# Kernel optimization log

Hardware: AMD Instinct MI355X
Metric: run time of the kernel (lower is better)

The kernel has to match this reference:

```python
import jax, jax.numpy as jnp
import numpy as np

VOXEL_SIZE = 0.4
STRIDE = 2
NUM_BATCH = 4
PRE_MAXSIZE = 1024  # nms_premaxsize
NMS_THR = 0.1
NEG_INF = -1e9


def setup_inputs() -> dict:
    key = jax.random.key(0)
    ks = jax.random.split(key, 7)
    N, C = 200000, 256
    feat = jax.random.normal(ks[0], (N, C), dtype=jnp.float32)
    batch_idx = jax.random.randint(ks[1], (N,), 0, NUM_BATCH, dtype=jnp.int32)
    coor = jax.random.randint(ks[2], (N, 2), 0, 400, dtype=jnp.int32)
    W_cls = jax.random.normal(ks[3], (C, 2), dtype=jnp.float32) * 0.02
    b_cls = jnp.zeros((2,), dtype=jnp.float32)
    W_reg = jax.random.normal(ks[4], (C, 9), dtype=jnp.float32) * 0.02
    b_reg = jnp.zeros((9,), dtype=jnp.float32)
    return {"feat": feat, "batch_idx": batch_idx, "coor": coor,
            "W_cls": W_cls, "b_cls": b_cls, "W_reg": W_reg, "b_reg": b_reg}


def _bev_iou(bx):
    # bx: [K,7] (x,y,z,l,w,h,r); axis-aligned BEV IoU on (x,y,l,w)
    x, y, l, w = bx[:, 0], bx[:, 1], bx[:, 3], bx[:, 4]
    x1, x2 = x - l / 2, x + l / 2
    y1, y2 = y - w / 2, y + w / 2
    ix = jnp.maximum(jnp.minimum(x2[:, None], x2[None, :]) - jnp.maximum(x1[:, None], x1[None, :]), 0.0)
    iy = jnp.maximum(jnp.minimum(y2[:, None], y2[None, :]) - jnp.maximum(y1[:, None], y1[None, :]), 0.0)
    inter = ix * iy
    area = l * w
    union = area[:, None] + area[None, :] - inter
    return inter / jnp.maximum(union, 1e-6)


def _nms_keep(iou):
    # greedy NMS over score-descending rows; returns keep mask [K]
    K = iou.shape[0]
    idx = jnp.arange(K)

    def body(i, supp):
        keep_i = jnp.logical_not(supp[i])
        new = keep_i & (iou[i] > NMS_THR) & (idx > i)
        return supp | new

    supp = jax.lax.fori_loop(0, K, body, jnp.zeros((K,), dtype=bool))
    return jnp.logical_not(supp)


def reference(feat, batch_idx, coor, W_cls, b_cls, W_reg, b_reg):
    # ---- shared heads over all sparse voxels ----
    cls_logits = feat @ W_cls + b_cls            # [N, 1+1] (neg evidence, class)
    probs = jax.nn.softmax(cls_logits, axis=-1)
    cls_prob = probs[:, 1:]                      # [N, n_cls]
    conf = jnp.max(cls_prob, axis=-1)            # [N]
    label = jnp.argmax(cls_prob, axis=-1)        # [N]

    reg = feat @ W_reg + b_reg                   # [N, 9] -> ctr(3) dim(3) dir(2) scr(1)
    ctr, dim, drn, scr = reg[:, :3], reg[:, 3:6], reg[:, 6:8], reg[:, 8]
    scr = jax.nn.sigmoid(scr)                    # sigmoid_keys=['scr']

    # indices2metric: voxel indices -> metric centers
    centers = coor.astype(jnp.float32) * (VOXEL_SIZE * STRIDE)  # [N, 2]

    xy = centers + ctr[:, :2]
    z = ctr[:, 2]
    lwh = jnp.exp(jnp.clip(dim, -6.0, 6.0))
    angle = jnp.arctan2(drn[:, 0], drn[:, 1])
    boxes = jnp.concatenate([xy, z[:, None], lwh, angle[:, None]], axis=-1)  # [N, 7]
    score = conf * scr                           # [N]

    def per_sample(b):
        s = jnp.where(batch_idx == b, score, NEG_INF)
        vals, idx = jax.lax.top_k(s, PRE_MAXSIZE)          # score-sorted (desc)
        bx = boxes[idx]                                     # [K, 7]
        lb = label[idx]                                     # [K]
        valid = vals > NEG_INF / 2
        iou = _bev_iou(bx)
        keep = _nms_keep(iou) & valid
        out = jnp.concatenate([bx, vals[:, None]], axis=-1) * keep[:, None]  # [K, 8]
        return out, lb, keep

    out, lb, keep = jax.vmap(per_sample)(jnp.arange(NUM_BATCH))
    return out, lb, keep
```

## Files before the change

### kernel.cpp

```cpp
#include <hip/hip_runtime.h>
#include <math.h>

#define NBATCH 4
#define PRE 1024
#define CAND 4096
#define NHIST 65536
#define MAXSLOT 384

typedef __attribute__((address_space(1))) const void GlbVoid;
typedef __attribute__((address_space(3))) void LdsVoid;

__device__ __forceinline__ void gld_lds16(const void* g, void* l) {
    __builtin_amdgcn_global_load_lds((GlbVoid*)g, (LdsVoid*)l, 16, 0, 0);
}

__device__ __forceinline__ unsigned long long allow_mask(int i, int l) {
    int base = l << 6;
    if (i < base) return ~0ull;
    int sh = i - base + 1;
    if (sh >= 64) return 0ull;
    return (~0ull) << sh;
}

__global__ void k0_weights(const float* __restrict__ Wcls, const float* __restrict__ bcls,
                           const float* __restrict__ Wreg, const float* __restrict__ breg,
                           double* __restrict__ Wd3, float* __restrict__ Wf8,
                           double* __restrict__ biasD, float* __restrict__ biasF) {
    int j = blockIdx.x;
    int c = threadIdx.x;
    if (j < 2) {
        Wd3[j * 256 + c] = (double)Wcls[c * 2 + j];
        if (c == 0) biasD[j] = (double)bcls[j];
    } else if (j == 10) {
        Wd3[2 * 256 + c] = (double)Wreg[c * 9 + 8];
        if (c == 0) biasD[2] = (double)breg[8];
    } else {
        int r = j - 2;
        Wf8[r * 256 + c] = Wreg[c * 9 + r];
        if (c == 0) biasF[r] = breg[r];
    }
}

__global__ __launch_bounds__(256) void k1_points(
    const float* __restrict__ feat, const int* __restrict__ batch_idx,
    const int* __restrict__ coor, const double* __restrict__ Wd3,
    const float* __restrict__ Wf8, const double* __restrict__ biasD,
    const float* __restrict__ biasF, float* __restrict__ pointData,
    unsigned long long* __restrict__ keys, unsigned int* __restrict__ hist, int N) {
    __shared__ float sbuf[2][256 * 32];
    const int tid = threadIdx.x;
    const int w = tid >> 6, lane = tid & 63;
    const int p0 = blockIdx.x * 256;

    double accD0 = 0.0, accD1 = 0.0, accD2 = 0.0;
    float accF[8];
#pragma unroll
    for (int j = 0; j < 8; ++j) accF[j] = 0.f;

    const int s_src = (lane & 7) ^ (lane >> 3);

    auto stage = [&](int buf, int ch) {
#pragma unroll
        for (int it = 0; it < 8; ++it) {
            int R0 = w * 64 + it * 8;
            int r = R0 + (lane >> 3);
            int gp = p0 + r;
            if (gp >= N) gp = N - 1;
            const float* g = feat + (size_t)gp * 256 + ch * 32 + s_src * 4;
            gld_lds16(g, &sbuf[buf][R0 * 32]);
        }
    };

    auto compute = [&](int buf, int ch) {
        const float* row = &sbuf[buf][tid * 32];
        const int rs = tid & 7;
#pragma unroll
        for (int k4 = 0; k4 < 8; ++k4) {
            const float4 v = *(const float4*)(row + ((k4 ^ rs) * 4));
            const int cb = ch * 32 + k4 * 4;
            float vv[4] = {v.x, v.y, v.z, v.w};
#pragma unroll
            for (int m = 0; m < 4; ++m) {
                int c = cb + m;
                double fd = (double)vv[m];
                accD0 = fma(fd, Wd3[c], accD0);
                accD1 = fma(fd, Wd3[256 + c], accD1);
                accD2 = fma(fd, Wd3[512 + c], accD2);
#pragma unroll
                for (int j = 0; j < 8; ++j) accF[j] = fmaf(vv[m], Wf8[j * 256 + c], accF[j]);
            }
        }
    };

    stage(0, 0);
    __syncthreads();
    for (int ch = 0; ch < 8; ++ch) {
        if (ch < 7) stage((ch + 1) & 1, ch + 1);
        compute(ch & 1, ch);
        __syncthreads();
    }

    int gp = p0 + tid;
    if (gp < N) {
        double d0 = biasD[0] + accD0, d1 = biasD[1] + accD1, d2 = biasD[2] + accD2;
        float f[8];
#pragma unroll
        for (int j = 0; j < 8; ++j) f[j] = biasF[j] + accF[j];
        double conf = 1.0 / (1.0 + exp(-(d1 - d0)));
        double scr = 1.0 / (1.0 + exp(-d2));
        double score = conf * scr;
        float s32 = (float)score;

        float cx = (float)coor[2 * gp] * 0.8f;
        float cy = (float)coor[2 * gp + 1] * 0.8f;
        float bx = cx + f[0], by = cy + f[1], bz = f[2];
        float bl = expf(fminf(fmaxf(f[3], -6.f), 6.f));
        float bw = expf(fminf(fmaxf(f[4], -6.f), 6.f));
        float bh = expf(fminf(fmaxf(f[5], -6.f), 6.f));
        float ba = atan2f(f[6], f[7]);

        float4* pd = (float4*)(pointData + (size_t)gp * 8);
        pd[0] = make_float4(bx, by, bz, bl);
        pd[1] = make_float4(bw, bh, ba, s32);
        keys[gp] = (unsigned long long)__double_as_longlong(score);
        int b = batch_idx[gp];
        atomicAdd(&hist[b * NHIST + (__float_as_uint(s32) >> 16)], 1u);
    }
}

__global__ __launch_bounds__(256) void k2_thresh(const unsigned int* __restrict__ hist,
                                                 unsigned int* __restrict__ Tarr) {
    int b = blockIdx.x, tid = threadIdx.x;
    __shared__ unsigned int csum[256];
    __shared__ unsigned int chunkv[256];
    __shared__ int stc;
    __shared__ unsigned int scum;
    const unsigned int* h = hist + b * NHIST;
    unsigned int s = 0;
    for (int m = 0; m < 256; ++m) s += h[tid * 256 + m];
    csum[tid] = s;
    __syncthreads();
    if (tid == 0) {
        unsigned int cum = 0; int tc = -1;
        for (int t = 255; t >= 0; --t) {
            if (cum + csum[t] >= 1024u) { tc = t; break; }
            cum += csum[t];
        }
        stc = tc; scum = cum;
    }
    __syncthreads();
    int tc = stc;
    if (tc < 0) { if (tid == 0) Tarr[b] = 0u; return; }
    chunkv[tid] = h[tc * 256 + tid];
    __syncthreads();
    if (tid == 0) {
        unsigned int cum = scum, T = (unsigned int)(tc * 256);
        for (int m = 255; m >= 0; --m) {
            unsigned int c = chunkv[m];
            if (cum + c >= 1024u) { T = (unsigned int)(tc * 256 + m); break; }
            cum += c;
        }
        Tarr[b] = T;
    }
}

__global__ void k3_compact(const int* __restrict__ batch_idx, const float* __restrict__ pointData,
                           const unsigned long long* __restrict__ keys,
                           const unsigned int* __restrict__ Tarr, unsigned int* __restrict__ candCount,
                           unsigned int* __restrict__ candIdx, unsigned long long* __restrict__ candKey,
                           int N) {
    int p = blockIdx.x * 256 + threadIdx.x;
    if (p >= N) return;
    int b = batch_idx[p];
    float s32 = pointData[(size_t)p * 8 + 7];
    unsigned int bucket = __float_as_uint(s32) >> 16;
    if (bucket >= Tarr[b]) {
        unsigned int pos = atomicAdd(&candCount[b], 1u);
        if (pos < CAND) {
            candIdx[b * CAND + pos] = (unsigned int)p;
            candKey[b * CAND + pos] = keys[p];
        }
    }
}

__global__ __launch_bounds__(1024) void k4_sort(const unsigned int* __restrict__ candCount,
                                                const unsigned int* __restrict__ candIdx,
                                                const unsigned long long* __restrict__ candKey,
                                                const float* __restrict__ pointData,
                                                float* __restrict__ topBox,
                                                unsigned int* __restrict__ validArr) {
    int b = blockIdx.x, tid = threadIdx.x;
    __shared__ unsigned long long ka[CAND];
    __shared__ unsigned int id[CAND];
    unsigned int cnt = candCount[b];
    if (cnt > CAND) cnt = CAND;
    int n = (cnt <= 2048u) ? 2048 : 4096;
    for (int t = tid; t < n; t += 1024) {
        if ((unsigned int)t < cnt) {
            ka[t] = ~candKey[b * CAND + t];
            id[t] = candIdx[b * CAND + t];
        } else {
            ka[t] = ~0ull;
            id[t] = 0xFFFFFFFFu;
        }
    }
    __syncthreads();
    for (int k = 2; k <= n; k <<= 1) {
        for (int j = k >> 1; j > 0; j >>= 1) {
            for (int t = tid; t < n; t += 1024) {
                int l = t ^ j;
                if (l > t) {
                    bool up = ((t & k) == 0);
                    unsigned long long kt = ka[t], kl = ka[l];
                    unsigned int it_ = id[t], il = id[l];
                    bool gt = (kt > kl) || (kt == kl && it_ > il);
                    if (gt == up) { ka[t] = kl; ka[l] = kt; id[t] = il; id[l] = it_; }
                }
            }
            __syncthreads();
        }
    }
    unsigned int gi = id[tid];
    bool valid = (gi != 0xFFFFFFFFu) && ((unsigned int)tid < cnt);
    float v[8];
#pragma unroll
    for (int k = 0; k < 8; ++k) v[k] = 0.f;
    if (valid) {
        const float* pd = pointData + (size_t)gi * 8;
#pragma unroll
        for (int k = 0; k < 8; ++k) v[k] = pd[k];
    }
    float* tb = topBox + (size_t)(b * PRE + tid) * 8;
#pragma unroll
    for (int k = 0; k < 8; ++k) tb[k] = v[k];
    validArr[b * PRE + tid] = valid ? 1u : 0u;
}

__global__ __launch_bounds__(256) void k5_iou(const float* __restrict__ topBox,
                                              unsigned long long* __restrict__ M) {
    int wid = blockIdx.x * 4 + (threadIdx.x >> 6);
    int lane = threadIdx.x & 63;
    int b = wid >> 14;
    int rem = wid & 16383;
    int i = rem >> 4;
    int wj = rem & 15;
    if (wj < (i >> 6)) return;
    const float* bi = topBox + (size_t)(b * PRE + i) * 8;
    int j = wj * 64 + lane;
    const float* bj = topBox + (size_t)(b * PRE + j) * 8;
    float xi = bi[0], yi = bi[1], li = bi[3], wi_ = bi[4];
    float xj = bj[0], yj = bj[1], lj = bj[3], wj_ = bj[4];
    float x1i = xi - li * 0.5f, x2i = xi + li * 0.5f;
    float y1i = yi - wi_ * 0.5f, y2i = yi + wi_ * 0.5f;
    float x1j = xj - lj * 0.5f, x2j = xj + lj * 0.5f;
    float y1j = yj - wj_ * 0.5f, y2j = yj + wj_ * 0.5f;
    float ix = fmaxf(fminf(x2i, x2j) - fmaxf(x1i, x1j), 0.0f);
    float iy = fmaxf(fminf(y2i, y2j) - fmaxf(y1i, y1j), 0.0f);
    float inter = ix * iy;
    float ai = li * wi_, aj = lj * wj_;
    float uni = ai + aj - inter;
    float iou = inter / fmaxf(uni, 1e-6f);
    unsigned long long m = __ballot(iou > 0.1f);
    if (lane == 0) M[(size_t)(b * PRE + i) * 16 + wj] = m;
}

__global__ __launch_bounds__(256) void k6_nms(const unsigned long long* __restrict__ M,
                                              const unsigned int* __restrict__ validArr,
                                              const float* __restrict__ topBox,
                                              float* __restrict__ out0,
                                              float* __restrict__ keepOut) {
    __shared__ unsigned long long Mc[MAXSLOT * 16];
    __shared__ unsigned int slotIdx[PRE];
    __shared__ unsigned int cntSh;
    __shared__ unsigned long long suppSh[16];
    int b = blockIdx.x, tid = threadIdx.x;
    if (tid == 0) cntSh = 0;
    __syncthreads();
    for (int r = tid; r < PRE; r += 256) {
        const unsigned long long* row = M + (size_t)(b * PRE + r) * 16;
        unsigned long long w[16];
        unsigned long long o = 0ull;
#pragma unroll
        for (int l = 0; l < 16; ++l) { w[l] = row[l] & allow_mask(r, l); o |= w[l]; }
        unsigned int s = 0xFFFFFFFFu;
        if (o != 0ull) {
            unsigned int slot = atomicAdd(&cntSh, 1u);
            if (slot < MAXSLOT) {
                s = slot;
#pragma unroll
                for (int l = 0; l < 16; ++l) Mc[slot * 16 + l] = w[l];
            } else s = 0xFFFFFFFEu;
        }
        slotIdx[r] = s;
    }
    __syncthreads();
    if (tid < 64) {
        int lane = tid;
        unsigned long long supp = 0ull;
        for (int g = 0; g < 16; ++g) {
            unsigned long long act = __ballot(slotIdx[g * 64 + lane] != 0xFFFFFFFFu);
            while (act) {
                int bit = __builtin_ctzll(act);
                act &= act - 1ull;
                int i = g * 64 + bit;
                unsigned long long wsup = __shfl(supp, g);
                bool keep_i = ((wsup >> (i & 63)) & 1ull) == 0ull;
                if (keep_i && lane < 16) {
                    unsigned int s = slotIdx[i];
                    unsigned long long add = (s < MAXSLOT)
                        ? Mc[s * 16 + lane]
                        : (M[(size_t)(b * PRE + i) * 16 + lane] & allow_mask(i, lane));
                    supp |= add;
                }
            }
        }
        if (lane < 16) suppSh[lane] = supp;
    }
    __syncthreads();
    for (int r = tid; r < PRE; r += 256) {
        bool keep = (((suppSh[r >> 6] >> (r & 63)) & 1ull) == 0ull) && (validArr[b * PRE + r] != 0u);
        float kf = keep ? 1.0f : 0.0f;
        const float* tb = topBox + (size_t)(b * PRE + r) * 8;
        float* o = out0 + (size_t)(b * PRE + r) * 8;
#pragma unroll
        for (int k = 0; k < 8; ++k) o[k] = tb[k] * kf;
        keepOut[b * PRE + r] = kf;
    }
}

extern "C" void kernel_launch(void* const* d_in, const int* in_sizes, int n_in,
                              void* d_out, int out_size, void* d_ws, size_t ws_size,
                              hipStream_t stream) {
    int N = in_sizes[0] / 256;
    const float* feat = (const float*)d_in[0];
    const int* batch_idx = (const int*)d_in[1];
    const int* coor = (const int*)d_in[2];
    const float* Wcls = (const float*)d_in[3];
    const float* bcls = (const float*)d_in[4];
    const float* Wreg = (const float*)d_in[5];
    const float* breg = (const float*)d_in[6];

    char* ws = (char*)d_ws;
    size_t off = 0;
    auto take = [&](size_t bytes) -> char* {
        char* r = ws + off;
        off += (bytes + 255) & ~(size_t)255;
        return r;
    };
    float* pointData = (float*)take((size_t)N * 8 * 4);
    unsigned long long* keys = (unsigned long long*)take((size_t)N * 8);
    unsigned int* hist = (unsigned int*)take((size_t)NBATCH * NHIST * 4);
    unsigned int* Tarr = (unsigned int*)take(NBATCH * 4);
    unsigned int* candCount = (unsigned int*)take(NBATCH * 4);
    unsigned int* candIdx = (unsigned int*)take(NBATCH * CAND * 4);
    unsigned long long* candKey = (unsigned long long*)take(NBATCH * CAND * 8);
    float* topBox = (float*)take(NBATCH * PRE * 8 * 4);
    unsigned int* validArr = (unsigned int*)take(NBATCH * PRE * 4);
    unsigned long long* M = (unsigned long long*)take((size_t)NBATCH * PRE * 16 * 8);
    double* Wd3 = (double*)take(3 * 256 * 8);
    float* Wf8 = (float*)take(8 * 256 * 4);
    double* biasD = (double*)take(3 * 8);
    float* biasF = (float*)take(8 * 4);

    float* out0 = (float*)d_out;
    float* keepOut = out0 + NBATCH * PRE * 8 + NBATCH * PRE;

    hipMemsetAsync(d_out, 0, (size_t)out_size * 4, stream);
    hipMemsetAsync(hist, 0, (size_t)NBATCH * NHIST * 4, stream);
    hipMemsetAsync(candCount, 0, NBATCH * 4, stream);

    int pbPts = (N + 255) / 256;
    k0_weights<<<dim3(11), dim3(256), 0, stream>>>(Wcls, bcls, Wreg, breg, Wd3, Wf8, biasD, biasF);
    k1_points<<<dim3(pbPts), dim3(256), 0, stream>>>(feat, batch_idx, coor,
                                                     Wd3, Wf8, biasD, biasF,
                                                     pointData, keys, hist, N);
    k2_thresh<<<dim3(NBATCH), dim3(256), 0, stream>>>(hist, Tarr);
    k3_compact<<<dim3(pbPts), dim3(256), 0, stream>>>(batch_idx, pointData, keys, Tarr,
                                                      candCount, candIdx, candKey, N);
    k4_sort<<<dim3(NBATCH), dim3(1024), 0, stream>>>(candCount, candIdx, candKey,
                                                     pointData, topBox, validArr);
    k5_iou<<<dim3(NBATCH * PRE * 16 / 4), dim3(256), 0, stream>>>(topBox, M);
    k6_nms<<<dim3(NBATCH), dim3(256), 0, stream>>>(M, validArr, topBox, out0, keepOut);
}
```

Baseline: 470.0 us.

## Use per-wave LDS staging without block barriers and merge memsets

```diff
diff --git a/kernel.cpp b/kernel.cpp
--- a/kernel.cpp
+++ b/kernel.cpp
@@ -47,7 +47,7 @@
     const float* __restrict__ Wf8, const double* __restrict__ biasD,
     const float* __restrict__ biasF, float* __restrict__ pointData,
     unsigned long long* __restrict__ keys, unsigned int* __restrict__ hist, int N) {
-    __shared__ float sbuf[2][256 * 32];
+    __shared__ float sbuf[4][2][64 * 16];
     const int tid = threadIdx.x;
     const int w = tid >> 6, lane = tid & 63;
     const int p0 = blockIdx.x * 256;
@@ -57,27 +57,26 @@
 #pragma unroll
     for (int j = 0; j < 8; ++j) accF[j] = 0.f;
 
-    const int s_src = (lane & 7) ^ (lane >> 3);
+    const int s_src = (lane & 3) ^ ((lane >> 3) & 3);
 
     auto stage = [&](int buf, int ch) {
 #pragma unroll
-        for (int it = 0; it < 8; ++it) {
-            int R0 = w * 64 + it * 8;
-            int r = R0 + (lane >> 3);
-            int gp = p0 + r;
+        for (int it = 0; it < 4; ++it) {
+            int r = it * 16 + (lane >> 2);
+            int gp = p0 + w * 64 + r;
             if (gp >= N) gp = N - 1;
-            const float* g = feat + (size_t)gp * 256 + ch * 32 + s_src * 4;
-            gld_lds16(g, &sbuf[buf][R0 * 32]);
+            const float* g = feat + (size_t)gp * 256 + ch * 16 + s_src * 4;
+            gld_lds16(g, &sbuf[w][buf][it * 256]);
         }
     };
 
     auto compute = [&](int buf, int ch) {
-        const float* row = &sbuf[buf][tid * 32];
-        const int rs = tid & 7;
-#pragma unroll
-        for (int k4 = 0; k4 < 8; ++k4) {
-            const float4 v = *(const float4*)(row + ((k4 ^ rs) * 4));
-            const int cb = ch * 32 + k4 * 4;
+        const float* row = &sbuf[w][buf][lane * 16];
+        const int rx = (lane >> 1) & 3;
+#pragma unroll
+        for (int s = 0; s < 4; ++s) {
+            const float4 v = *(const float4*)(row + ((s ^ rx) * 4));
+            const int cb = ch * 16 + s * 4;
             float vv[4] = {v.x, v.y, v.z, v.w};
 #pragma unroll
             for (int m = 0; m < 4; ++m) {
@@ -93,12 +92,15 @@
     };
 
     stage(0, 0);
-    __syncthreads();
-    for (int ch = 0; ch < 8; ++ch) {
-        if (ch < 7) stage((ch + 1) & 1, ch + 1);
+    for (int ch = 0; ch < 15; ++ch) {
+        stage((ch + 1) & 1, ch + 1);
+        asm volatile("s_waitcnt vmcnt(4)" ::: "memory");
+        __builtin_amdgcn_sched_barrier(0);
         compute(ch & 1, ch);
-        __syncthreads();
-    }
+    }
+    asm volatile("s_waitcnt vmcnt(0)" ::: "memory");
+    __builtin_amdgcn_sched_barrier(0);
+    compute(1, 15);
 
     int gp = p0 + tid;
     if (gp < N) {
@@ -350,8 +352,8 @@
     float* pointData = (float*)take((size_t)N * 8 * 4);
     unsigned long long* keys = (unsigned long long*)take((size_t)N * 8);
     unsigned int* hist = (unsigned int*)take((size_t)NBATCH * NHIST * 4);
+    unsigned int* candCount = (unsigned int*)take(NBATCH * 4);
     unsigned int* Tarr = (unsigned int*)take(NBATCH * 4);
-    unsigned int* candCount = (unsigned int*)take(NBATCH * 4);
     unsigned int* candIdx = (unsigned int*)take(NBATCH * CAND * 4);
     unsigned long long* candKey = (unsigned long long*)take(NBATCH * CAND * 8);
     float* topBox = (float*)take(NBATCH * PRE * 8 * 4);
@@ -366,8 +368,7 @@
     float* keepOut = out0 + NBATCH * PRE * 8 + NBATCH * PRE;
 
     hipMemsetAsync(d_out, 0, (size_t)out_size * 4, stream);
-    hipMemsetAsync(hist, 0, (size_t)NBATCH * NHIST * 4, stream);
-    hipMemsetAsync(candCount, 0, NBATCH * 4, stream);
+    hipMemsetAsync(hist, 0, (size_t)NBATCH * NHIST * 4 + NBATCH * 4, stream);
 
     int pbPts = (N + 255) / 256;
     k0_weights<<<dim3(11), dim3(256), 0, stream>>>(Wcls, bcls, Wreg, breg, Wd3, Wf8, biasD, biasF);
```

New measurement: 483.8 us. 1.03x slower.

## Replace LDS-staged feature loads with direct per-thread float4 loads; merge memsets

Applied to the files above, without the earlier changes.

```diff
diff --git a/kernel.cpp b/kernel.cpp
--- a/kernel.cpp
+++ b/kernel.cpp
@@ -6,13 +6,6 @@
 #define CAND 4096
 #define NHIST 65536
 #define MAXSLOT 384
-
-typedef __attribute__((address_space(1))) const void GlbVoid;
-typedef __attribute__((address_space(3))) void LdsVoid;
-
-__device__ __forceinline__ void gld_lds16(const void* g, void* l) {
-    __builtin_amdgcn_global_load_lds((GlbVoid*)g, (LdsVoid*)l, 16, 0, 0);
-}
 
 __device__ __forceinline__ unsigned long long allow_mask(int i, int l) {
     int base = l << 6;
@@ -47,85 +40,60 @@
     const float* __restrict__ Wf8, const double* __restrict__ biasD,
     const float* __restrict__ biasF, float* __restrict__ pointData,
     unsigned long long* __restrict__ keys, unsigned int* __restrict__ hist, int N) {
-    __shared__ float sbuf[2][256 * 32];
-    const int tid = threadIdx.x;
-    const int w = tid >> 6, lane = tid & 63;
-    const int p0 = blockIdx.x * 256;
+    const int gp = blockIdx.x * 256 + threadIdx.x;
+    if (gp >= N) return;
+    const float4* fp = (const float4*)(feat + (size_t)gp * 256);
 
     double accD0 = 0.0, accD1 = 0.0, accD2 = 0.0;
     float accF[8];
 #pragma unroll
     for (int j = 0; j < 8; ++j) accF[j] = 0.f;
 
-    const int s_src = (lane & 7) ^ (lane >> 3);
-
-    auto stage = [&](int buf, int ch) {
-#pragma unroll
-        for (int it = 0; it < 8; ++it) {
-            int R0 = w * 64 + it * 8;
-            int r = R0 + (lane >> 3);
-            int gp = p0 + r;
-            if (gp >= N) gp = N - 1;
-            const float* g = feat + (size_t)gp * 256 + ch * 32 + s_src * 4;
-            gld_lds16(g, &sbuf[buf][R0 * 32]);
-        }
-    };
-
-    auto compute = [&](int buf, int ch) {
-        const float* row = &sbuf[buf][tid * 32];
-        const int rs = tid & 7;
-#pragma unroll
-        for (int k4 = 0; k4 < 8; ++k4) {
-            const float4 v = *(const float4*)(row + ((k4 ^ rs) * 4));
-            const int cb = ch * 32 + k4 * 4;
-            float vv[4] = {v.x, v.y, v.z, v.w};
+#pragma unroll 2
+    for (int it = 0; it < 8; ++it) {
+        float4 v[8];
+#pragma unroll
+        for (int j = 0; j < 8; ++j) v[j] = fp[it * 8 + j];
+#pragma unroll
+        for (int j = 0; j < 8; ++j) {
+            const int c = it * 32 + j * 4;
+            const float vv[4] = {v[j].x, v[j].y, v[j].z, v[j].w};
 #pragma unroll
             for (int m = 0; m < 4; ++m) {
-                int c = cb + m;
-                double fd = (double)vv[m];
-                accD0 = fma(fd, Wd3[c], accD0);
-                accD1 = fma(fd, Wd3[256 + c], accD1);
-                accD2 = fma(fd, Wd3[512 + c], accD2);
-#pragma unroll
-                for (int j = 0; j < 8; ++j) accF[j] = fmaf(vv[m], Wf8[j * 256 + c], accF[j]);
+                const double fd = (double)vv[m];
+                accD0 = fma(fd, Wd3[c + m], accD0);
+                accD1 = fma(fd, Wd3[256 + c + m], accD1);
+                accD2 = fma(fd, Wd3[512 + c + m], accD2);
+#pragma unroll
+                for (int jj = 0; jj < 8; ++jj)
+                    accF[jj] = fmaf(vv[m], Wf8[jj * 256 + c + m], accF[jj]);
             }
         }
-    };
-
-    stage(0, 0);
-    __syncthreads();
-    for (int ch = 0; ch < 8; ++ch) {
-        if (ch < 7) stage((ch + 1) & 1, ch + 1);
-        compute(ch & 1, ch);
-        __syncthreads();
-    }
-
-    int gp = p0 + tid;
-    if (gp < N) {
-        double d0 = biasD[0] + accD0, d1 = biasD[1] + accD1, d2 = biasD[2] + accD2;
-        float f[8];
-#pragma unroll
-        for (int j = 0; j < 8; ++j) f[j] = biasF[j] + accF[j];
-        double conf = 1.0 / (1.0 + exp(-(d1 - d0)));
-        double scr = 1.0 / (1.0 + exp(-d2));
-        double score = conf * scr;
-        float s32 = (float)score;
-
-        float cx = (float)coor[2 * gp] * 0.8f;
-        float cy = (float)coor[2 * gp + 1] * 0.8f;
-        float bx = cx + f[0], by = cy + f[1], bz = f[2];
-        float bl = expf(fminf(fmaxf(f[3], -6.f), 6.f));
-        float bw = expf(fminf(fmaxf(f[4], -6.f), 6.f));
-        float bh = expf(fminf(fmaxf(f[5], -6.f), 6.f));
-        float ba = atan2f(f[6], f[7]);
-
-        float4* pd = (float4*)(pointData + (size_t)gp * 8);
-        pd[0] = make_float4(bx, by, bz, bl);
-        pd[1] = make_float4(bw, bh, ba, s32);
-        keys[gp] = (unsigned long long)__double_as_longlong(score);
-        int b = batch_idx[gp];
-        atomicAdd(&hist[b * NHIST + (__float_as_uint(s32) >> 16)], 1u);
-    }
+    }
+
+    double d0 = biasD[0] + accD0, d1 = biasD[1] + accD1, d2 = biasD[2] + accD2;
+    float f[8];
+#pragma unroll
+    for (int j = 0; j < 8; ++j) f[j] = biasF[j] + accF[j];
+    double conf = 1.0 / (1.0 + exp(-(d1 - d0)));
+    double scr = 1.0 / (1.0 + exp(-d2));
+    double score = conf * scr;
+    float s32 = (float)score;
+
+    float cx = (float)coor[2 * gp] * 0.8f;
+    float cy = (float)coor[2 * gp + 1] * 0.8f;
+    float bx = cx + f[0], by = cy + f[1], bz = f[2];
+    float bl = expf(fminf(fmaxf(f[3], -6.f), 6.f));
+    float bw = expf(fminf(fmaxf(f[4], -6.f), 6.f));
+    float bh = expf(fminf(fmaxf(f[5], -6.f), 6.f));
+    float ba = atan2f(f[6], f[7]);
+
+    float4* pd = (float4*)(pointData + (size_t)gp * 8);
+    pd[0] = make_float4(bx, by, bz, bl);
+    pd[1] = make_float4(bw, bh, ba, s32);
+    keys[gp] = (unsigned long long)__double_as_longlong(score);
+    int b = batch_idx[gp];
+    atomicAdd(&hist[b * NHIST + (__float_as_uint(s32) >> 16)], 1u);
 }
 
 __global__ __launch_bounds__(256) void k2_thresh(const unsigned int* __restrict__ hist,
@@ -350,8 +318,8 @@
     float* pointData = (float*)take((size_t)N * 8 * 4);
     unsigned long long* keys = (unsigned long long*)take((size_t)N * 8);
     unsigned int* hist = (unsigned int*)take((size_t)NBATCH * NHIST * 4);
+    unsigned int* candCount = (unsigned int*)take(NBATCH * 4);
     unsigned int* Tarr = (unsigned int*)take(NBATCH * 4);
-    unsigned int* candCount = (unsigned int*)take(NBATCH * 4);
     unsigned int* candIdx = (unsigned int*)take(NBATCH * CAND * 4);
     unsigned long long* candKey = (unsigned long long*)take(NBATCH * CAND * 8);
     float* topBox = (float*)take(NBATCH * PRE * 8 * 4);
@@ -366,8 +334,7 @@
     float* keepOut = out0 + NBATCH * PRE * 8 + NBATCH * PRE;
 
     hipMemsetAsync(d_out, 0, (size_t)out_size * 4, stream);
-    hipMemsetAsync(hist, 0, (size_t)NBATCH * NHIST * 4, stream);
-    hipMemsetAsync(candCount, 0, NBATCH * 4, stream);
+    hipMemsetAsync(hist, 0, (size_t)NBATCH * NHIST * 4 + NBATCH * 4, stream);
 
     int pbPts = (N + 255) / 256;
     k0_weights<<<dim3(11), dim3(256), 0, stream>>>(Wcls, bcls, Wreg, breg, Wd3, Wf8, biasD, biasF);
```

New measurement: 488.8 us. 1.04x slower.

## Pack float score and index into one 64-bit sort key

Applied to the files above, without the earlier changes.

```diff
diff --git a/kernel.cpp b/kernel.cpp
--- a/kernel.cpp
+++ b/kernel.cpp
@@ -46,7 +46,7 @@
     const int* __restrict__ coor, const double* __restrict__ Wd3,
     const float* __restrict__ Wf8, const double* __restrict__ biasD,
     const float* __restrict__ biasF, float* __restrict__ pointData,
-    unsigned long long* __restrict__ keys, unsigned int* __restrict__ hist, int N) {
+    unsigned int* __restrict__ hist, int N) {
     __shared__ float sbuf[2][256 * 32];
     const int tid = threadIdx.x;
     const int w = tid >> 6, lane = tid & 63;
@@ -122,7 +122,6 @@
         float4* pd = (float4*)(pointData + (size_t)gp * 8);
         pd[0] = make_float4(bx, by, bz, bl);
         pd[1] = make_float4(bw, bh, ba, s32);
-        keys[gp] = (unsigned long long)__double_as_longlong(score);
         int b = batch_idx[gp];
         atomicAdd(&hist[b * NHIST + (__float_as_uint(s32) >> 16)], 1u);
     }
@@ -165,45 +164,33 @@
 }
 
 __global__ void k3_compact(const int* __restrict__ batch_idx, const float* __restrict__ pointData,
-                           const unsigned long long* __restrict__ keys,
                            const unsigned int* __restrict__ Tarr, unsigned int* __restrict__ candCount,
-                           unsigned int* __restrict__ candIdx, unsigned long long* __restrict__ candKey,
-                           int N) {
+                           unsigned long long* __restrict__ candKey, int N) {
     int p = blockIdx.x * 256 + threadIdx.x;
     if (p >= N) return;
     int b = batch_idx[p];
     float s32 = pointData[(size_t)p * 8 + 7];
-    unsigned int bucket = __float_as_uint(s32) >> 16;
-    if (bucket >= Tarr[b]) {
+    unsigned int sb = __float_as_uint(s32);
+    if ((sb >> 16) >= Tarr[b]) {
         unsigned int pos = atomicAdd(&candCount[b], 1u);
         if (pos < CAND) {
-            candIdx[b * CAND + pos] = (unsigned int)p;
-            candKey[b * CAND + pos] = keys[p];
+            candKey[b * CAND + pos] = ((unsigned long long)(~sb) << 32) | (unsigned int)p;
         }
     }
 }
 
 __global__ __launch_bounds__(1024) void k4_sort(const unsigned int* __restrict__ candCount,
-                                                const unsigned int* __restrict__ candIdx,
                                                 const unsigned long long* __restrict__ candKey,
                                                 const float* __restrict__ pointData,
                                                 float* __restrict__ topBox,
                                                 unsigned int* __restrict__ validArr) {
     int b = blockIdx.x, tid = threadIdx.x;
     __shared__ unsigned long long ka[CAND];
-    __shared__ unsigned int id[CAND];
     unsigned int cnt = candCount[b];
     if (cnt > CAND) cnt = CAND;
     int n = (cnt <= 2048u) ? 2048 : 4096;
-    for (int t = tid; t < n; t += 1024) {
-        if ((unsigned int)t < cnt) {
-            ka[t] = ~candKey[b * CAND + t];
-            id[t] = candIdx[b * CAND + t];
-        } else {
-            ka[t] = ~0ull;
-            id[t] = 0xFFFFFFFFu;
-        }
-    }
+    for (int t = tid; t < n; t += 1024)
+        ka[t] = ((unsigned int)t < cnt) ? candKey[b * CAND + t] : ~0ull;
     __syncthreads();
     for (int k = 2; k <= n; k <<= 1) {
         for (int j = k >> 1; j > 0; j >>= 1) {
@@ -212,16 +199,15 @@
                 if (l > t) {
                     bool up = ((t & k) == 0);
                     unsigned long long kt = ka[t], kl = ka[l];
-                    unsigned int it_ = id[t], il = id[l];
-                    bool gt = (kt > kl) || (kt == kl && it_ > il);
-                    if (gt == up) { ka[t] = kl; ka[l] = kt; id[t] = il; id[l] = it_; }
+                    if ((kt > kl) == up) { ka[t] = kl; ka[l] = kt; }
                 }
             }
             __syncthreads();
         }
     }
-    unsigned int gi = id[tid];
-    bool valid = (gi != 0xFFFFFFFFu) && ((unsigned int)tid < cnt);
+    unsigned long long kt = ka[tid];
+    unsigned int gi = (unsigned int)kt;
+    bool valid = ((unsigned int)tid < cnt) && (gi != 0xFFFFFFFFu);
     float v[8];
 #pragma unroll
     for (int k = 0; k < 8; ++k) v[k] = 0.f;
@@ -348,11 +334,9 @@
         return r;
     };
     float* pointData = (float*)take((size_t)N * 8 * 4);
-    unsigned long long* keys = (unsigned long long*)take((size_t)N * 8);
     unsigned int* hist = (unsigned int*)take((size_t)NBATCH * NHIST * 4);
+    unsigned int* candCount = (unsigned int*)take(NBATCH * 4);
     unsigned int* Tarr = (unsigned int*)take(NBATCH * 4);
-    unsigned int* candCount = (unsigned int*)take(NBATCH * 4);
-    unsigned int* candIdx = (unsigned int*)take(NBATCH * CAND * 4);
     unsigned long long* candKey = (unsigned long long*)take(NBATCH * CAND * 8);
     float* topBox = (float*)take(NBATCH * PRE * 8 * 4);
     unsigned int* validArr = (unsigned int*)take(NBATCH * PRE * 4);
@@ -366,18 +350,17 @@
     float* keepOut = out0 + NBATCH * PRE * 8 + NBATCH * PRE;
 
     hipMemsetAsync(d_out, 0, (size_t)out_size * 4, stream);
-    hipMemsetAsync(hist, 0, (size_t)NBATCH * NHIST * 4, stream);
-    hipMemsetAsync(candCount, 0, NBATCH * 4, stream);
+    hipMemsetAsync(hist, 0, (size_t)NBATCH * NHIST * 4 + NBATCH * 4, stream);
 
     int pbPts = (N + 255) / 256;
     k0_weights<<<dim3(11), dim3(256), 0, stream>>>(Wcls, bcls, Wreg, breg, Wd3, Wf8, biasD, biasF);
     k1_points<<<dim3(pbPts), dim3(256), 0, stream>>>(feat, batch_idx, coor,
                                                      Wd3, Wf8, biasD, biasF,
-                                                     pointData, keys, hist, N);
+                                                     pointData, hist, N);
     k2_thresh<<<dim3(NBATCH), dim3(256), 0, stream>>>(hist, Tarr);
-    k3_compact<<<dim3(pbPts), dim3(256), 0, stream>>>(batch_idx, pointData, keys, Tarr,
-                                                      candCount, candIdx, candKey, N);
-    k4_sort<<<dim3(NBATCH), dim3(1024), 0, stream>>>(candCount, candIdx, candKey,
+    k3_compact<<<dim3(pbPts), dim3(256), 0, stream>>>(batch_idx, pointData, Tarr,
+                                                      candCount, candKey, N);
+    k4_sort<<<dim3(NBATCH), dim3(1024), 0, stream>>>(candCount, candKey,
                                                      pointData, topBox, validArr);
     k5_iou<<<dim3(NBATCH * PRE * 16 / 4), dim3(256), 0, stream>>>(topBox, M);
     k6_nms<<<dim3(NBATCH), dim3(256), 0, stream>>>(M, validArr, topBox, out0, keepOut);
```

Result: faster. 457.5 us (-2.7%).
